# Kernel tuning notes

Hardware: AMD Instinct MI355X
Metric: run time of the kernel (lower is better)

Reference implementation:

```python
import jax, jax.numpy as jnp
import numpy as np

B, H, S, D = 4, 16, 1024, 64


def setup_inputs() -> dict:
    key = jax.random.key(0)
    kq, kk, kv, kw = jax.random.split(key, 4)
    xq = jax.random.normal(kq, (B, H, S, D), dtype=jnp.float32)
    xk = jax.random.normal(kk, (B, H, S, D), dtype=jnp.float32)
    xv = jax.random.normal(kv, (B, H, S, D), dtype=jnp.float32)
    # wpsm: nn.Linear(n_heads, n_heads, bias=False) weight, shape [H_out, H_in]
    bound = 1.0 / np.sqrt(H)
    W = jax.random.uniform(kw, (H, H), minval=-bound, maxval=bound, dtype=jnp.float32)
    return {"xq": xq, "xk": xk, "xv": xv, "W": W, "causal": 1}


def reference(xq, xk, xv, W, causal):
    head_dim = xq.shape[-1]
    sq, sk = xq.shape[-2], xk.shape[-2]
    # QK^T scaled: [B, H, Sq, Sk]
    scores = jnp.einsum("bhqd,bhkd->bhqk", xq, xk) * jax.lax.rsqrt(jnp.float32(head_dim))
    # head-mixing linear over head axis: mixed[b,g,q,k] = sum_h W[g,h] * scores[b,h,q,k]
    scores = jnp.einsum("gh,bhqk->bgqk", W, scores)
    if causal:
        mask = jnp.triu(jnp.full((sq, sk), -jnp.inf, dtype=scores.dtype), k=1)
        scores = scores + mask  # broadcast over [B, H]
    probs = jax.nn.softmax(scores.astype(jnp.float32), axis=-1).astype(xq.dtype)
    out = jnp.einsum("bhqk,bhkd->bhqd", probs, xv)
    return out.transpose(0, 2, 1, 3)  # [B, Sq, H, D]
```

## Files before the change

### kernel.cpp

```cpp
#include <hip/hip_runtime.h>
#include <math.h>

#define NB 4
#define HH 16
#define SS 1024
#define DD 64
#define NKST 16

typedef __attribute__((ext_vector_type(8))) short bf16x8;
typedef __attribute__((ext_vector_type(4))) float f32x4;

static __device__ __forceinline__ short f2bf(float f) {
    __bf16 h = (__bf16)f;
    return __builtin_bit_cast(short, h);
}
static __device__ __forceinline__ float bflo(int w) {
    return __builtin_bit_cast(float, (unsigned)w << 16);
}
static __device__ __forceinline__ float bfhi(int w) {
    return __builtin_bit_cast(float, (unsigned)w & 0xffff0000u);
}
static __device__ __forceinline__ float bfu(unsigned short u) {
    return __builtin_bit_cast(float, (unsigned)u << 16);
}
static __device__ __forceinline__ int pidx(int pos, int hp) {
    int s = ((pos >> 2) & 3) | (((pos >> 9) & 1) << 2);
    return pos * 8 + (hp ^ s);
}
static __device__ __forceinline__ int midx(int g, int loc, int x3) {
    return g * 512 + ((((loc >> 2) ^ x3) << 2) | (loc & 3));
}

static __device__ __forceinline__ bf16x8 load8_bf16(const float* p) {
    const float4* p4 = reinterpret_cast<const float4*>(p);
    float4 a = p4[0], b = p4[1];
    bf16x8 f;
    f[0]=f2bf(a.x); f[1]=f2bf(a.y); f[2]=f2bf(a.z); f[3]=f2bf(a.w);
    f[4]=f2bf(b.x); f[5]=f2bf(b.y); f[6]=f2bf(b.z); f[7]=f2bf(b.w);
    return f;
}

__global__ __launch_bounds__(256) void prep_kfrag(const float* __restrict__ xk,
                                                  short* __restrict__ kfr) {
    int c = blockIdx.x * 256 + threadIdx.x;
    int lane = c & 63, ds = (c >> 6) & 1, kt = (c >> 7) & 3;
    int kst = (c >> 9) & 15, h = (c >> 13) & 15, b = c >> 17;
    const float* src = xk + ((size_t)((b * HH + h) * SS) + kst * 64 + kt * 16 + (lane & 15)) * DD
                          + ds * 32 + (lane >> 4) * 8;
    *(reinterpret_cast<bf16x8*>(kfr) + c) = load8_bf16(src);
}

__global__ __launch_bounds__(256) void prep_vfrag(const float* __restrict__ xv,
                                                  short* __restrict__ vfr) {
    __shared__ float T[64][65];
    int tile = blockIdx.x;
    int t = threadIdx.x;
    const float* src = xv + ((size_t)(tile >> 4) * SS + (tile & 15) * 64) * DD;
    int row = t >> 2, col = (t & 3) * 16;
#pragma unroll
    for (int ii = 0; ii < 4; ++ii) {
        float4 v = *reinterpret_cast<const float4*>(src + row * DD + col + ii * 4);
        T[row][col + ii*4] = v.x; T[row][col + ii*4 + 1] = v.y;
        T[row][col + ii*4 + 2] = v.z; T[row][col + ii*4 + 3] = v.w;
    }
    __syncthreads();
#pragma unroll
    for (int jj = 0; jj < 2; ++jj) {
        int c2 = t * 2 + jj;
        int lane = c2 & 63, nt = (c2 >> 6) & 3, kc = (c2 >> 8) & 1;
        bf16x8 o;
#pragma unroll
        for (int i = 0; i < 8; ++i)
            o[i] = f2bf(T[kc * 32 + (lane >> 4) * 8 + i][nt * 16 + (lane & 15)]);
        *(reinterpret_cast<bf16x8*>(vfr) + (size_t)tile * 512 + c2) = o;
    }
}

__global__ __launch_bounds__(1024, 1) void hca_fused(
    const float* __restrict__ xq, const short* __restrict__ kfr,
    const short* __restrict__ vfr, const float* __restrict__ Wm,
    const int* __restrict__ causalp, unsigned short* __restrict__ ppO,
    float2* __restrict__ ppml)
{
    __shared__ int Pbuf[8192];
    __shared__ int Mbuf[8192];

    const int tid  = threadIdx.x;
    const int lane = tid & 63;
    const int w    = tid >> 6;
    const int l15  = lane & 15;
    const int lg   = lane >> 4;

    const int bid  = blockIdx.x;
    const int b    = bid & 3;
    const int pp   = (bid >> 2) & 31;
    const int kpar = (bid >> 7) & 1;

    const int causal = causalp[0];
    const int hp = w & 7;
    const int kh = w >> 3;
    const int g  = w;

    const float LOG2E = 1.44269504088896f;

    bf16x8 wt = {0,0,0,0,0,0,0,0};
    if (lg < 2) {
#pragma unroll
        for (int ii = 0; ii < 8; ++ii)
            wt[ii] = f2bf(Wm[l15 * 16 + lg * 8 + ii] * 0.125f * LOG2E);
    }

    const short* vb0 = vfr + (size_t)(b * HH + g) * NKST * 8 * 512 + lane * 8;
    const short* kb0 = kfr + (size_t)(b * HH + 2 * hp) * NKST * 8 * 512 + lane * 8;

#pragma unroll 1
    for (int seg = 0; seg < 2; ++seg) {
        const int qt = seg ? pp : 63 - pp;
        const int q0 = qt << 4;
        const int pairIdx = b * 64 + qt;

        bf16x8 qf[2][2];
#pragma unroll
        for (int hi = 0; hi < 2; ++hi) {
            const float* qp = xq + ((size_t)(b * HH + 2 * hp + hi) * SS + q0 + l15) * DD + lg * 8;
#pragma unroll
            for (int ds = 0; ds < 2; ++ds) qf[hi][ds] = load8_bf16(qp + ds * 32);
        }

        f32x4 oacc[4];
#pragma unroll
        for (int nt = 0; nt < 4; ++nt) oacc[nt] = (f32x4){0.f, 0.f, 0.f, 0.f};
        float mrun = -INFINITY, lrun = 0.f;

        const int nkf = causal ? ((q0 + 16 + 63) >> 6) : NKST;

#pragma unroll 1
        for (int kst = kpar; kst < nkf; kst += 2) {
            const int k0 = kst << 6;

            const short* kbase = kb0 + (size_t)kst * 8 * 512;
            __builtin_amdgcn_s_setprio(1);
#pragma unroll
            for (int kt2 = 0; kt2 < 2; ++kt2) {
                const int kt = kh * 2 + kt2;
                f32x4 a0 = (f32x4){0.f,0.f,0.f,0.f}, a1 = a0;
#pragma unroll
                for (int ds = 0; ds < 2; ++ds) {
                    bf16x8 kfa = *reinterpret_cast<const bf16x8*>(kbase + (kt*2 + ds) * 512);
                    bf16x8 kfb = *reinterpret_cast<const bf16x8*>(kbase + (NKST*8 + kt*2 + ds) * 512);
                    a0 = __builtin_amdgcn_mfma_f32_16x16x32_bf16(qf[0][ds], kfa, a0, 0, 0, 0);
                    a1 = __builtin_amdgcn_mfma_f32_16x16x32_bf16(qf[1][ds], kfb, a1, 0, 0, 0);
                }
#pragma unroll
                for (int r = 0; r < 4; ++r) {
                    int pos = (lg * 4 + r) * 64 + kt * 16 + l15;
                    int pk = (int)(unsigned short)f2bf(a0[r]) | ((int)(unsigned short)f2bf(a1[r]) << 16);
                    Pbuf[pidx(pos, hp)] = pk;
                }
            }
            __builtin_amdgcn_s_setprio(0);

            const short* vbase = vb0 + (size_t)kst * 8 * 512;
            bf16x8 vf[8];
#pragma unroll
            for (int kc = 0; kc < 2; ++kc)
#pragma unroll
                for (int nt = 0; nt < 4; ++nt)
                    vf[kc * 4 + nt] = *reinterpret_cast<const bf16x8*>(vbase + (kc*4 + nt) * 512);

            __syncthreads();

#pragma unroll
            for (int m = 0; m < 4; ++m) {
                const int c = w * 4 + m;
                const int pos = c * 16 + l15;
                int4 ia = {0, 0, 0, 0};
                if (lg < 2) {
                    ia.x = Pbuf[pidx(pos, lg * 4 + 0)];
                    ia.y = Pbuf[pidx(pos, lg * 4 + 1)];
                    ia.z = Pbuf[pidx(pos, lg * 4 + 2)];
                    ia.w = Pbuf[pidx(pos, lg * 4 + 3)];
                }
                bf16x8 A = __builtin_bit_cast(bf16x8, ia);
                f32x4 cc = (f32x4){0.f, 0.f, 0.f, 0.f};
                cc = __builtin_amdgcn_mfma_f32_16x16x32_bf16(A, wt, cc, 0, 0, 0);
                int loc = w * 32 + (c & 3) * 8 + lg * 2;
                int x3 = (w + l15) & 7;
                int u0 = (int)(unsigned short)f2bf(cc[0]) | ((int)(unsigned short)f2bf(cc[1]) << 16);
                int u1 = (int)(unsigned short)f2bf(cc[2]) | ((int)(unsigned short)f2bf(cc[3]) << 16);
                *reinterpret_cast<int2*>(&Mbuf[midx(l15, loc, x3)]) = make_int2(u0, u1);
            }
            __syncthreads();

            const int x3r = (l15 + g) & 7;
            int4 rA = *reinterpret_cast<const int4*>(&Mbuf[midx(g, l15 * 32 + lg * 4, x3r)]);
            int4 rB = *reinterpret_cast<const int4*>(&Mbuf[midx(g, l15 * 32 + 16 + lg * 4, x3r)]);

            float sm[16];
#pragma unroll
            for (int jj = 0; jj < 4; ++jj) {
                sm[2*jj]     = bflo(rA[jj]);  sm[2*jj + 1] = bfhi(rA[jj]);
                sm[8 + 2*jj] = bflo(rB[jj]);  sm[9 + 2*jj] = bfhi(rB[jj]);
            }
            if (causal && kst == nkf - 1) {
#pragma unroll
                for (int jj = 0; jj < 16; ++jj) {
                    int kk = (jj < 8) ? (lg * 8 + jj) : (32 + lg * 8 + (jj - 8));
                    if (k0 + kk > q0 + l15) sm[jj] = -INFINITY;
                }
            }

            float mx[4];
#pragma unroll
            for (int t = 0; t < 4; ++t)
                mx[t] = fmaxf(fmaxf(sm[4*t], sm[4*t+1]), fmaxf(sm[4*t+2], sm[4*t+3]));
            float mt = fmaxf(fmaxf(mx[0], mx[1]), fmaxf(mx[2], mx[3]));
            mt = fmaxf(mt, __shfl_xor(mt, 16));
            mt = fmaxf(mt, __shfl_xor(mt, 32));

            if (__any(mt > mrun + 8.0f)) {
                float mnew = fmaxf(mrun, mt);
                float scl = __builtin_amdgcn_exp2f(mrun - mnew);
                mrun = mnew;
                lrun *= scl;
                int scli = __builtin_bit_cast(int, scl);
#pragma unroll
                for (int r = 0; r < 4; ++r) {
                    int v = __builtin_amdgcn_ds_bpermute((lg * 4 + r) * 4, scli);
                    float s = __builtin_bit_cast(float, v);
#pragma unroll
                    for (int nt = 0; nt < 4; ++nt) oacc[nt][r] *= s;
                }
            }

#pragma unroll
            for (int jj = 0; jj < 16; ++jj) sm[jj] = __builtin_amdgcn_exp2f(sm[jj] - mrun);
            float s0 = ((sm[0]+sm[1]) + (sm[2]+sm[3])) + ((sm[4]+sm[5]) + (sm[6]+sm[7]));
            float s1 = ((sm[8]+sm[9]) + (sm[10]+sm[11])) + ((sm[12]+sm[13]) + (sm[14]+sm[15]));
            lrun += s0 + s1;

            int paw[8];
#pragma unroll
            for (int t = 0; t < 8; ++t)
                paw[t] = (int)(unsigned short)f2bf(sm[2*t]) | ((int)(unsigned short)f2bf(sm[2*t+1]) << 16);
            bf16x8 pa0 = __builtin_bit_cast(bf16x8, *(int4*)&paw[0]);
            bf16x8 pa1 = __builtin_bit_cast(bf16x8, *(int4*)&paw[4]);

            __builtin_amdgcn_s_setprio(1);
#pragma unroll
            for (int nt = 0; nt < 4; ++nt) {
                oacc[nt] = __builtin_amdgcn_mfma_f32_16x16x32_bf16(pa0, vf[nt], oacc[nt], 0, 0, 0);
                oacc[nt] = __builtin_amdgcn_mfma_f32_16x16x32_bf16(pa1, vf[4 + nt], oacc[nt], 0, 0, 0);
            }
            __builtin_amdgcn_s_setprio(0);
        }

        float lt = lrun;
        lt += __shfl_xor(lt, 16);
        lt += __shfl_xor(lt, 32);
        if (lg == 0)
            ppml[(((size_t)pairIdx * 2 + kpar) * 16 + g) * 16 + l15] = make_float2(mrun, lt);
        float rl = (lt > 0.f) ? (1.0f / lt) : 0.f;
        int rli = __builtin_bit_cast(int, rl);
        size_t obase = (((size_t)pairIdx * 2 + kpar) * 16 + g) * 1024;
#pragma unroll
        for (int r = 0; r < 4; ++r) {
            int v = __builtin_amdgcn_ds_bpermute((lg * 4 + r) * 4, rli);
            float linv = __builtin_bit_cast(float, v);
            int q = lg * 4 + r;
#pragma unroll
            for (int nt = 0; nt < 4; ++nt)
                ppO[obase + q * 64 + nt * 16 + l15] =
                    (unsigned short)f2bf(oacc[nt][r] * linv);
        }
        __syncthreads();
    }
}

__global__ __launch_bounds__(256) void hca_combine(
    const unsigned short* __restrict__ ppO, const float2* __restrict__ ppml,
    float* __restrict__ out)
{
    const int pairIdx = blockIdx.x;
    const int b = pairIdx >> 6, qt = pairIdx & 63;
    const int t = threadIdx.x;
    const int g = t >> 4, dc = t & 15;

    const size_t o0 = (((size_t)pairIdx * 2 + 0) * 16 + g) * 1024;
    const size_t o1 = (((size_t)pairIdx * 2 + 1) * 16 + g) * 1024;
    const float2* ml0p = ppml + (((size_t)pairIdx * 2 + 0) * 16 + g) * 16;
    const float2* ml1p = ppml + (((size_t)pairIdx * 2 + 1) * 16 + g) * 16;

#pragma unroll 4
    for (int q = 0; q < 16; ++q) {
        float2 ml0 = ml0p[q], ml1 = ml1p[q];
        float ms = fmaxf(ml0.x, ml1.x);
        float w0 = ml0.y * exp2f(ml0.x - ms);
        float w1 = ml1.y * exp2f(ml1.x - ms);
        float rs = 1.0f / (w0 + w1);
        float a0 = w0 * rs, a1 = w1 * rs;
        ushort4 u0 = *reinterpret_cast<const ushort4*>(ppO + o0 + q * 64 + dc * 4);
        ushort4 u1 = *reinterpret_cast<const ushort4*>(ppO + o1 + q * 64 + dc * 4);
        float4 res;
        res.x = a0 * bfu(u0.x) + a1 * bfu(u1.x);
        res.y = a0 * bfu(u0.y) + a1 * bfu(u1.y);
        res.z = a0 * bfu(u0.z) + a1 * bfu(u1.z);
        res.w = a0 * bfu(u0.w) + a1 * bfu(u1.w);
        *reinterpret_cast<float4*>(out + (((size_t)b * SS + qt * 16 + q) * HH + g) * DD + dc * 4) = res;
    }
}

extern "C" void kernel_launch(void* const* d_in, const int* in_sizes, int n_in,
                              void* d_out, int out_size, void* d_ws, size_t ws_size,
                              hipStream_t stream) {
    const float* xq = (const float*)d_in[0];
    const float* xk = (const float*)d_in[1];
    const float* xv = (const float*)d_in[2];
    const float* Wm = (const float*)d_in[3];
    const int* causal = (const int*)d_in[4];
    float* out = (float*)d_out;

    short* vfr = (short*)d_ws;
    short* kfr = vfr + (size_t)NB * HH * SS * DD;
    unsigned short* ppO = (unsigned short*)(kfr + (size_t)NB * HH * SS * DD);
    float2* ppml = (float2*)(ppO + (size_t)512 * 16 * 1024);

    prep_kfrag<<<2048, 256, 0, stream>>>(xk, kfr);
    prep_vfrag<<<NB * HH * NKST, 256, 0, stream>>>(xv, vfr);

    hca_fused<<<256, 1024, 0, stream>>>(xq, kfr, vfr, Wm, causal, ppO, ppml);
    hca_combine<<<256, 256, 0, stream>>>(ppO, ppml, out);
}
```

Before: 78.42 us.

## Merge K/V prep kernels and software-prefetch K fragments across loop iterations

Folds the two preprocessing kernels into one launch that branches on block index, which removes one kernel launch and its gap. In the main fused kernel, the K fragments for the next key step are loaded into registers before the current step's softmax and PV work, so global load latency overlaps with compute. V fragment loads are split into two halves, with the second half issued after the second barrier to shorten live ranges. The change adds register pressure in a kernel capped at 1024 threads per block, and the last iteration issues a redundant reload.

```diff
diff --git a/kernel.cpp b/kernel.cpp
--- a/kernel.cpp
+++ b/kernel.cpp
@@ -40,39 +40,41 @@
     return f;
 }
 
-__global__ __launch_bounds__(256) void prep_kfrag(const float* __restrict__ xk,
-                                                  short* __restrict__ kfr) {
-    int c = blockIdx.x * 256 + threadIdx.x;
-    int lane = c & 63, ds = (c >> 6) & 1, kt = (c >> 7) & 3;
-    int kst = (c >> 9) & 15, h = (c >> 13) & 15, b = c >> 17;
-    const float* src = xk + ((size_t)((b * HH + h) * SS) + kst * 64 + kt * 16 + (lane & 15)) * DD
-                          + ds * 32 + (lane >> 4) * 8;
-    *(reinterpret_cast<bf16x8*>(kfr) + c) = load8_bf16(src);
-}
-
-__global__ __launch_bounds__(256) void prep_vfrag(const float* __restrict__ xv,
-                                                  short* __restrict__ vfr) {
+__global__ __launch_bounds__(256) void prep_all(const float* __restrict__ xk,
+                                                short* __restrict__ kfr,
+                                                const float* __restrict__ xv,
+                                                short* __restrict__ vfr) {
     __shared__ float T[64][65];
-    int tile = blockIdx.x;
-    int t = threadIdx.x;
-    const float* src = xv + ((size_t)(tile >> 4) * SS + (tile & 15) * 64) * DD;
-    int row = t >> 2, col = (t & 3) * 16;
-#pragma unroll
-    for (int ii = 0; ii < 4; ++ii) {
-        float4 v = *reinterpret_cast<const float4*>(src + row * DD + col + ii * 4);
-        T[row][col + ii*4] = v.x; T[row][col + ii*4 + 1] = v.y;
-        T[row][col + ii*4 + 2] = v.z; T[row][col + ii*4 + 3] = v.w;
-    }
-    __syncthreads();
-#pragma unroll
-    for (int jj = 0; jj < 2; ++jj) {
-        int c2 = t * 2 + jj;
-        int lane = c2 & 63, nt = (c2 >> 6) & 3, kc = (c2 >> 8) & 1;
-        bf16x8 o;
-#pragma unroll
-        for (int i = 0; i < 8; ++i)
-            o[i] = f2bf(T[kc * 32 + (lane >> 4) * 8 + i][nt * 16 + (lane & 15)]);
-        *(reinterpret_cast<bf16x8*>(vfr) + (size_t)tile * 512 + c2) = o;
+    const int bid = blockIdx.x;
+    const int t = threadIdx.x;
+    if (bid < 2048) {
+        int c = bid * 256 + t;
+        int lane = c & 63, ds = (c >> 6) & 1, kt = (c >> 7) & 3;
+        int kst = (c >> 9) & 15, h = (c >> 13) & 15, b = c >> 17;
+        const float* src = xk + ((size_t)((b * HH + h) * SS) + kst * 64 + kt * 16 + (lane & 15)) * DD
+                              + ds * 32 + (lane >> 4) * 8;
+        *(reinterpret_cast<bf16x8*>(kfr) + c) = load8_bf16(src);
+    } else {
+        int tile = bid - 2048;
+        const float* src = xv + ((size_t)(tile >> 4) * SS + (tile & 15) * 64) * DD;
+        int row = t >> 2, col = (t & 3) * 16;
+#pragma unroll
+        for (int ii = 0; ii < 4; ++ii) {
+            float4 v = *reinterpret_cast<const float4*>(src + row * DD + col + ii * 4);
+            T[row][col + ii*4] = v.x; T[row][col + ii*4 + 1] = v.y;
+            T[row][col + ii*4 + 2] = v.z; T[row][col + ii*4 + 3] = v.w;
+        }
+        __syncthreads();
+#pragma unroll
+        for (int jj = 0; jj < 2; ++jj) {
+            int c2 = t * 2 + jj;
+            int lane = c2 & 63, nt = (c2 >> 6) & 3, kc = (c2 >> 8) & 1;
+            bf16x8 o;
+#pragma unroll
+            for (int i = 0; i < 8; ++i)
+                o[i] = f2bf(T[kc * 32 + (lane >> 4) * 8 + i][nt * 16 + (lane & 15)]);
+            *(reinterpret_cast<bf16x8*>(vfr) + (size_t)tile * 512 + c2) = o;
+        }
     }
 }
 
@@ -134,11 +136,23 @@
 
         const int nkf = causal ? ((q0 + 16 + 63) >> 6) : NKST;
 
+        bf16x8 kA[2][2], kB[2][2];
+        {
+            const short* kbase = kb0 + (size_t)kpar * 8 * 512;
+#pragma unroll
+            for (int kt2 = 0; kt2 < 2; ++kt2)
+#pragma unroll
+                for (int ds = 0; ds < 2; ++ds) {
+                    const int kt = kh * 2 + kt2;
+                    kA[kt2][ds] = *reinterpret_cast<const bf16x8*>(kbase + (kt*2 + ds) * 512);
+                    kB[kt2][ds] = *reinterpret_cast<const bf16x8*>(kbase + (NKST*8 + kt*2 + ds) * 512);
+                }
+        }
+
 #pragma unroll 1
         for (int kst = kpar; kst < nkf; kst += 2) {
             const int k0 = kst << 6;
 
-            const short* kbase = kb0 + (size_t)kst * 8 * 512;
             __builtin_amdgcn_s_setprio(1);
 #pragma unroll
             for (int kt2 = 0; kt2 < 2; ++kt2) {
@@ -146,10 +160,8 @@
                 f32x4 a0 = (f32x4){0.f,0.f,0.f,0.f}, a1 = a0;
 #pragma unroll
                 for (int ds = 0; ds < 2; ++ds) {
-                    bf16x8 kfa = *reinterpret_cast<const bf16x8*>(kbase + (kt*2 + ds) * 512);
-                    bf16x8 kfb = *reinterpret_cast<const bf16x8*>(kbase + (NKST*8 + kt*2 + ds) * 512);
-                    a0 = __builtin_amdgcn_mfma_f32_16x16x32_bf16(qf[0][ds], kfa, a0, 0, 0, 0);
-                    a1 = __builtin_amdgcn_mfma_f32_16x16x32_bf16(qf[1][ds], kfb, a1, 0, 0, 0);
+                    a0 = __builtin_amdgcn_mfma_f32_16x16x32_bf16(qf[0][ds], kA[kt2][ds], a0, 0, 0, 0);
+                    a1 = __builtin_amdgcn_mfma_f32_16x16x32_bf16(qf[1][ds], kB[kt2][ds], a1, 0, 0, 0);
                 }
 #pragma unroll
                 for (int r = 0; r < 4; ++r) {
@@ -160,13 +172,23 @@
             }
             __builtin_amdgcn_s_setprio(0);
 
+            {
+                const int kstn = (kst + 2 < nkf) ? (kst + 2) : kst;
+                const short* kbase = kb0 + (size_t)kstn * 8 * 512;
+#pragma unroll
+                for (int kt2 = 0; kt2 < 2; ++kt2)
+#pragma unroll
+                    for (int ds = 0; ds < 2; ++ds) {
+                        const int kt = kh * 2 + kt2;
+                        kA[kt2][ds] = *reinterpret_cast<const bf16x8*>(kbase + (kt*2 + ds) * 512);
+                        kB[kt2][ds] = *reinterpret_cast<const bf16x8*>(kbase + (NKST*8 + kt*2 + ds) * 512);
+                    }
+            }
             const short* vbase = vb0 + (size_t)kst * 8 * 512;
-            bf16x8 vf[8];
-#pragma unroll
-            for (int kc = 0; kc < 2; ++kc)
-#pragma unroll
-                for (int nt = 0; nt < 4; ++nt)
-                    vf[kc * 4 + nt] = *reinterpret_cast<const bf16x8*>(vbase + (kc*4 + nt) * 512);
+            bf16x8 vf0[4];
+#pragma unroll
+            for (int nt = 0; nt < 4; ++nt)
+                vf0[nt] = *reinterpret_cast<const bf16x8*>(vbase + nt * 512);
 
             __syncthreads();
 
@@ -192,6 +214,11 @@
             }
             __syncthreads();
 
+            bf16x8 vf1[4];
+#pragma unroll
+            for (int nt = 0; nt < 4; ++nt)
+                vf1[nt] = *reinterpret_cast<const bf16x8*>(vbase + (4 + nt) * 512);
+
             const int x3r = (l15 + g) & 7;
             int4 rA = *reinterpret_cast<const int4*>(&Mbuf[midx(g, l15 * 32 + lg * 4, x3r)]);
             int4 rB = *reinterpret_cast<const int4*>(&Mbuf[midx(g, l15 * 32 + 16 + lg * 4, x3r)]);
@@ -248,10 +275,11 @@
 
             __builtin_amdgcn_s_setprio(1);
 #pragma unroll
-            for (int nt = 0; nt < 4; ++nt) {
-                oacc[nt] = __builtin_amdgcn_mfma_f32_16x16x32_bf16(pa0, vf[nt], oacc[nt], 0, 0, 0);
-                oacc[nt] = __builtin_amdgcn_mfma_f32_16x16x32_bf16(pa1, vf[4 + nt], oacc[nt], 0, 0, 0);
-            }
+            for (int nt = 0; nt < 4; ++nt)
+                oacc[nt] = __builtin_amdgcn_mfma_f32_16x16x32_bf16(pa0, vf0[nt], oacc[nt], 0, 0, 0);
+#pragma unroll
+            for (int nt = 0; nt < 4; ++nt)
+                oacc[nt] = __builtin_amdgcn_mfma_f32_16x16x32_bf16(pa1, vf1[nt], oacc[nt], 0, 0, 0);
             __builtin_amdgcn_s_setprio(0);
         }
 
@@ -325,8 +353,7 @@
     unsigned short* ppO = (unsigned short*)(kfr + (size_t)NB * HH * SS * DD);
     float2* ppml = (float2*)(ppO + (size_t)512 * 16 * 1024);
 
-    prep_kfrag<<<2048, 256, 0, stream>>>(xk, kfr);
-    prep_vfrag<<<NB * HH * NKST, 256, 0, stream>>>(xv, vfr);
+    prep_all<<<2048 + NB * HH * NKST, 256, 0, stream>>>(xk, kfr, xv, vfr);
 
     hca_fused<<<256, 1024, 0, stream>>>(xq, kfr, vfr, Wm, causal, ppO, ppml);
     hca_combine<<<256, 256, 0, stream>>>(ppO, ppml, out);
```

Measured after the change: 124.6 us. 58.9% more time.

## Split fused attention grid per query tile and merge K/V prep kernels

Applied to the files above, without the earlier changes.

The main kernel now launches 512 blocks, each handling one query tile, instead of 256 blocks that each looped over a balanced pair of tiles. The min-occupancy hint in the launch bounds is dropped so more than one block may be resident per CU. The K and V fragment prep kernels are merged into a single launch that branches on block index, saving one launch. The PV MFMAs are regrouped into two separate loops. Per-block causal work is now uneven, so load balance depends on the hardware scheduler and on register and LDS pressure allowing two blocks per CU.

```diff
diff --git a/kernel.cpp b/kernel.cpp
--- a/kernel.cpp
+++ b/kernel.cpp
@@ -40,43 +40,45 @@
     return f;
 }
 
-__global__ __launch_bounds__(256) void prep_kfrag(const float* __restrict__ xk,
-                                                  short* __restrict__ kfr) {
-    int c = blockIdx.x * 256 + threadIdx.x;
-    int lane = c & 63, ds = (c >> 6) & 1, kt = (c >> 7) & 3;
-    int kst = (c >> 9) & 15, h = (c >> 13) & 15, b = c >> 17;
-    const float* src = xk + ((size_t)((b * HH + h) * SS) + kst * 64 + kt * 16 + (lane & 15)) * DD
-                          + ds * 32 + (lane >> 4) * 8;
-    *(reinterpret_cast<bf16x8*>(kfr) + c) = load8_bf16(src);
-}
-
-__global__ __launch_bounds__(256) void prep_vfrag(const float* __restrict__ xv,
-                                                  short* __restrict__ vfr) {
+__global__ __launch_bounds__(256) void prep_all(const float* __restrict__ xk,
+                                                short* __restrict__ kfr,
+                                                const float* __restrict__ xv,
+                                                short* __restrict__ vfr) {
     __shared__ float T[64][65];
-    int tile = blockIdx.x;
-    int t = threadIdx.x;
-    const float* src = xv + ((size_t)(tile >> 4) * SS + (tile & 15) * 64) * DD;
-    int row = t >> 2, col = (t & 3) * 16;
-#pragma unroll
-    for (int ii = 0; ii < 4; ++ii) {
-        float4 v = *reinterpret_cast<const float4*>(src + row * DD + col + ii * 4);
-        T[row][col + ii*4] = v.x; T[row][col + ii*4 + 1] = v.y;
-        T[row][col + ii*4 + 2] = v.z; T[row][col + ii*4 + 3] = v.w;
-    }
-    __syncthreads();
-#pragma unroll
-    for (int jj = 0; jj < 2; ++jj) {
-        int c2 = t * 2 + jj;
-        int lane = c2 & 63, nt = (c2 >> 6) & 3, kc = (c2 >> 8) & 1;
-        bf16x8 o;
-#pragma unroll
-        for (int i = 0; i < 8; ++i)
-            o[i] = f2bf(T[kc * 32 + (lane >> 4) * 8 + i][nt * 16 + (lane & 15)]);
-        *(reinterpret_cast<bf16x8*>(vfr) + (size_t)tile * 512 + c2) = o;
-    }
-}
-
-__global__ __launch_bounds__(1024, 1) void hca_fused(
+    const int bid = blockIdx.x;
+    const int t = threadIdx.x;
+    if (bid < 2048) {
+        int c = bid * 256 + t;
+        int lane = c & 63, ds = (c >> 6) & 1, kt = (c >> 7) & 3;
+        int kst = (c >> 9) & 15, h = (c >> 13) & 15, b = c >> 17;
+        const float* src = xk + ((size_t)((b * HH + h) * SS) + kst * 64 + kt * 16 + (lane & 15)) * DD
+                              + ds * 32 + (lane >> 4) * 8;
+        *(reinterpret_cast<bf16x8*>(kfr) + c) = load8_bf16(src);
+    } else {
+        int tile = bid - 2048;
+        const float* src = xv + ((size_t)(tile >> 4) * SS + (tile & 15) * 64) * DD;
+        int row = t >> 2, col = (t & 3) * 16;
+#pragma unroll
+        for (int ii = 0; ii < 4; ++ii) {
+            float4 v = *reinterpret_cast<const float4*>(src + row * DD + col + ii * 4);
+            T[row][col + ii*4] = v.x; T[row][col + ii*4 + 1] = v.y;
+            T[row][col + ii*4 + 2] = v.z; T[row][col + ii*4 + 3] = v.w;
+        }
+        __syncthreads();
+#pragma unroll
+        for (int jj = 0; jj < 2; ++jj) {
+            int c2 = t * 2 + jj;
+            int lane = c2 & 63, nt = (c2 >> 6) & 3, kc = (c2 >> 8) & 1;
+            bf16x8 o;
+#pragma unroll
+            for (int i = 0; i < 8; ++i)
+                o[i] = f2bf(T[kc * 32 + (lane >> 4) * 8 + i][nt * 16 + (lane & 15)]);
+            *(reinterpret_cast<bf16x8*>(vfr) + (size_t)tile * 512 + c2) = o;
+        }
+    }
+}
+
+__global__ __launch_bounds__(1024) void hca_fused(
     const float* __restrict__ xq, const short* __restrict__ kfr,
     const short* __restrict__ vfr, const float* __restrict__ Wm,
     const int* __restrict__ causalp, unsigned short* __restrict__ ppO,
@@ -93,8 +95,12 @@
 
     const int bid  = blockIdx.x;
     const int b    = bid & 3;
-    const int pp   = (bid >> 2) & 31;
-    const int kpar = (bid >> 7) & 1;
+    const int u    = (bid >> 2) & 63;
+    const int r    = (bid >> 8) & 1;
+    const int qt   = r ? u : 63 - u;
+    const int kpar = u & 1;
+    const int q0   = qt << 4;
+    const int pairIdx = b * 64 + qt;
 
     const int causal = causalp[0];
     const int hp = w & 7;
@@ -113,167 +119,160 @@
     const short* vb0 = vfr + (size_t)(b * HH + g) * NKST * 8 * 512 + lane * 8;
     const short* kb0 = kfr + (size_t)(b * HH + 2 * hp) * NKST * 8 * 512 + lane * 8;
 
+    bf16x8 qf[2][2];
+#pragma unroll
+    for (int hi = 0; hi < 2; ++hi) {
+        const float* qp = xq + ((size_t)(b * HH + 2 * hp + hi) * SS + q0 + l15) * DD + lg * 8;
+#pragma unroll
+        for (int ds = 0; ds < 2; ++ds) qf[hi][ds] = load8_bf16(qp + ds * 32);
+    }
+
+    f32x4 oacc[4];
+#pragma unroll
+    for (int nt = 0; nt < 4; ++nt) oacc[nt] = (f32x4){0.f, 0.f, 0.f, 0.f};
+    float mrun = -INFINITY, lrun = 0.f;
+
+    const int nkf = causal ? ((q0 + 16 + 63) >> 6) : NKST;
+
 #pragma unroll 1
-    for (int seg = 0; seg < 2; ++seg) {
-        const int qt = seg ? pp : 63 - pp;
-        const int q0 = qt << 4;
-        const int pairIdx = b * 64 + qt;
-
-        bf16x8 qf[2][2];
-#pragma unroll
-        for (int hi = 0; hi < 2; ++hi) {
-            const float* qp = xq + ((size_t)(b * HH + 2 * hp + hi) * SS + q0 + l15) * DD + lg * 8;
-#pragma unroll
-            for (int ds = 0; ds < 2; ++ds) qf[hi][ds] = load8_bf16(qp + ds * 32);
-        }
-
-        f32x4 oacc[4];
-#pragma unroll
-        for (int nt = 0; nt < 4; ++nt) oacc[nt] = (f32x4){0.f, 0.f, 0.f, 0.f};
-        float mrun = -INFINITY, lrun = 0.f;
-
-        const int nkf = causal ? ((q0 + 16 + 63) >> 6) : NKST;
-
-#pragma unroll 1
-        for (int kst = kpar; kst < nkf; kst += 2) {
-            const int k0 = kst << 6;
-
-            const short* kbase = kb0 + (size_t)kst * 8 * 512;
-            __builtin_amdgcn_s_setprio(1);
-#pragma unroll
-            for (int kt2 = 0; kt2 < 2; ++kt2) {
-                const int kt = kh * 2 + kt2;
-                f32x4 a0 = (f32x4){0.f,0.f,0.f,0.f}, a1 = a0;
-#pragma unroll
-                for (int ds = 0; ds < 2; ++ds) {
-                    bf16x8 kfa = *reinterpret_cast<const bf16x8*>(kbase + (kt*2 + ds) * 512);
-                    bf16x8 kfb = *reinterpret_cast<const bf16x8*>(kbase + (NKST*8 + kt*2 + ds) * 512);
-                    a0 = __builtin_amdgcn_mfma_f32_16x16x32_bf16(qf[0][ds], kfa, a0, 0, 0, 0);
-                    a1 = __builtin_amdgcn_mfma_f32_16x16x32_bf16(qf[1][ds], kfb, a1, 0, 0, 0);
-                }
-#pragma unroll
-                for (int r = 0; r < 4; ++r) {
-                    int pos = (lg * 4 + r) * 64 + kt * 16 + l15;
-                    int pk = (int)(unsigned short)f2bf(a0[r]) | ((int)(unsigned short)f2bf(a1[r]) << 16);
-                    Pbuf[pidx(pos, hp)] = pk;
-                }
-            }
-            __builtin_amdgcn_s_setprio(0);
-
-            const short* vbase = vb0 + (size_t)kst * 8 * 512;
-            bf16x8 vf[8];
-#pragma unroll
-            for (int kc = 0; kc < 2; ++kc)
-#pragma unroll
-                for (int nt = 0; nt < 4; ++nt)
-                    vf[kc * 4 + nt] = *reinterpret_cast<const bf16x8*>(vbase + (kc*4 + nt) * 512);
-
-            __syncthreads();
-
-#pragma unroll
-            for (int m = 0; m < 4; ++m) {
-                const int c = w * 4 + m;
-                const int pos = c * 16 + l15;
-                int4 ia = {0, 0, 0, 0};
-                if (lg < 2) {
-                    ia.x = Pbuf[pidx(pos, lg * 4 + 0)];
-                    ia.y = Pbuf[pidx(pos, lg * 4 + 1)];
-                    ia.z = Pbuf[pidx(pos, lg * 4 + 2)];
-                    ia.w = Pbuf[pidx(pos, lg * 4 + 3)];
-                }
-                bf16x8 A = __builtin_bit_cast(bf16x8, ia);
-                f32x4 cc = (f32x4){0.f, 0.f, 0.f, 0.f};
-                cc = __builtin_amdgcn_mfma_f32_16x16x32_bf16(A, wt, cc, 0, 0, 0);
-                int loc = w * 32 + (c & 3) * 8 + lg * 2;
-                int x3 = (w + l15) & 7;
-                int u0 = (int)(unsigned short)f2bf(cc[0]) | ((int)(unsigned short)f2bf(cc[1]) << 16);
-                int u1 = (int)(unsigned short)f2bf(cc[2]) | ((int)(unsigned short)f2bf(cc[3]) << 16);
-                *reinterpret_cast<int2*>(&Mbuf[midx(l15, loc, x3)]) = make_int2(u0, u1);
-            }
-            __syncthreads();
-
-            const int x3r = (l15 + g) & 7;
-            int4 rA = *reinterpret_cast<const int4*>(&Mbuf[midx(g, l15 * 32 + lg * 4, x3r)]);
-            int4 rB = *reinterpret_cast<const int4*>(&Mbuf[midx(g, l15 * 32 + 16 + lg * 4, x3r)]);
-
-            float sm[16];
-#pragma unroll
-            for (int jj = 0; jj < 4; ++jj) {
-                sm[2*jj]     = bflo(rA[jj]);  sm[2*jj + 1] = bfhi(rA[jj]);
-                sm[8 + 2*jj] = bflo(rB[jj]);  sm[9 + 2*jj] = bfhi(rB[jj]);
-            }
-            if (causal && kst == nkf - 1) {
-#pragma unroll
-                for (int jj = 0; jj < 16; ++jj) {
-                    int kk = (jj < 8) ? (lg * 8 + jj) : (32 + lg * 8 + (jj - 8));
-                    if (k0 + kk > q0 + l15) sm[jj] = -INFINITY;
-                }
-            }
-
-            float mx[4];
-#pragma unroll
-            for (int t = 0; t < 4; ++t)
-                mx[t] = fmaxf(fmaxf(sm[4*t], sm[4*t+1]), fmaxf(sm[4*t+2], sm[4*t+3]));
-            float mt = fmaxf(fmaxf(mx[0], mx[1]), fmaxf(mx[2], mx[3]));
-            mt = fmaxf(mt, __shfl_xor(mt, 16));
-            mt = fmaxf(mt, __shfl_xor(mt, 32));
-
-            if (__any(mt > mrun + 8.0f)) {
-                float mnew = fmaxf(mrun, mt);
-                float scl = __builtin_amdgcn_exp2f(mrun - mnew);
-                mrun = mnew;
-                lrun *= scl;
-                int scli = __builtin_bit_cast(int, scl);
-#pragma unroll
-                for (int r = 0; r < 4; ++r) {
-                    int v = __builtin_amdgcn_ds_bpermute((lg * 4 + r) * 4, scli);
-                    float s = __builtin_bit_cast(float, v);
-#pragma unroll
-                    for (int nt = 0; nt < 4; ++nt) oacc[nt][r] *= s;
-                }
-            }
-
-#pragma unroll
-            for (int jj = 0; jj < 16; ++jj) sm[jj] = __builtin_amdgcn_exp2f(sm[jj] - mrun);
-            float s0 = ((sm[0]+sm[1]) + (sm[2]+sm[3])) + ((sm[4]+sm[5]) + (sm[6]+sm[7]));
-            float s1 = ((sm[8]+sm[9]) + (sm[10]+sm[11])) + ((sm[12]+sm[13]) + (sm[14]+sm[15]));
-            lrun += s0 + s1;
-
-            int paw[8];
-#pragma unroll
-            for (int t = 0; t < 8; ++t)
-                paw[t] = (int)(unsigned short)f2bf(sm[2*t]) | ((int)(unsigned short)f2bf(sm[2*t+1]) << 16);
-            bf16x8 pa0 = __builtin_bit_cast(bf16x8, *(int4*)&paw[0]);
-            bf16x8 pa1 = __builtin_bit_cast(bf16x8, *(int4*)&paw[4]);
-
-            __builtin_amdgcn_s_setprio(1);
-#pragma unroll
-            for (int nt = 0; nt < 4; ++nt) {
-                oacc[nt] = __builtin_amdgcn_mfma_f32_16x16x32_bf16(pa0, vf[nt], oacc[nt], 0, 0, 0);
-                oacc[nt] = __builtin_amdgcn_mfma_f32_16x16x32_bf16(pa1, vf[4 + nt], oacc[nt], 0, 0, 0);
-            }
-            __builtin_amdgcn_s_setprio(0);
-        }
-
-        float lt = lrun;
-        lt += __shfl_xor(lt, 16);
-        lt += __shfl_xor(lt, 32);
-        if (lg == 0)
-            ppml[(((size_t)pairIdx * 2 + kpar) * 16 + g) * 16 + l15] = make_float2(mrun, lt);
-        float rl = (lt > 0.f) ? (1.0f / lt) : 0.f;
-        int rli = __builtin_bit_cast(int, rl);
-        size_t obase = (((size_t)pairIdx * 2 + kpar) * 16 + g) * 1024;
-#pragma unroll
-        for (int r = 0; r < 4; ++r) {
-            int v = __builtin_amdgcn_ds_bpermute((lg * 4 + r) * 4, rli);
-            float linv = __builtin_bit_cast(float, v);
-            int q = lg * 4 + r;
+    for (int kst = kpar; kst < nkf; kst += 2) {
+        const int k0 = kst << 6;
+
+        const short* kbase = kb0 + (size_t)kst * 8 * 512;
+        __builtin_amdgcn_s_setprio(1);
+#pragma unroll
+        for (int kt2 = 0; kt2 < 2; ++kt2) {
+            const int kt = kh * 2 + kt2;
+            f32x4 a0 = (f32x4){0.f,0.f,0.f,0.f}, a1 = a0;
+#pragma unroll
+            for (int ds = 0; ds < 2; ++ds) {
+                bf16x8 kfa = *reinterpret_cast<const bf16x8*>(kbase + (kt*2 + ds) * 512);
+                bf16x8 kfb = *reinterpret_cast<const bf16x8*>(kbase + (NKST*8 + kt*2 + ds) * 512);
+                a0 = __builtin_amdgcn_mfma_f32_16x16x32_bf16(qf[0][ds], kfa, a0, 0, 0, 0);
+                a1 = __builtin_amdgcn_mfma_f32_16x16x32_bf16(qf[1][ds], kfb, a1, 0, 0, 0);
+            }
+#pragma unroll
+            for (int rr = 0; rr < 4; ++rr) {
+                int pos = (lg * 4 + rr) * 64 + kt * 16 + l15;
+                int pk = (int)(unsigned short)f2bf(a0[rr]) | ((int)(unsigned short)f2bf(a1[rr]) << 16);
+                Pbuf[pidx(pos, hp)] = pk;
+            }
+        }
+        __builtin_amdgcn_s_setprio(0);
+
+        const short* vbase = vb0 + (size_t)kst * 8 * 512;
+        bf16x8 vf[8];
+#pragma unroll
+        for (int kc = 0; kc < 2; ++kc)
 #pragma unroll
             for (int nt = 0; nt < 4; ++nt)
-                ppO[obase + q * 64 + nt * 16 + l15] =
-                    (unsigned short)f2bf(oacc[nt][r] * linv);
-        }
+                vf[kc * 4 + nt] = *reinterpret_cast<const bf16x8*>(vbase + (kc*4 + nt) * 512);
+
         __syncthreads();
+
+#pragma unroll
+        for (int m = 0; m < 4; ++m) {
+            const int c = w * 4 + m;
+            const int pos = c * 16 + l15;
+            int4 ia = {0, 0, 0, 0};
+            if (lg < 2) {
+                ia.x = Pbuf[pidx(pos, lg * 4 + 0)];
+                ia.y = Pbuf[pidx(pos, lg * 4 + 1)];
+                ia.z = Pbuf[pidx(pos, lg * 4 + 2)];
+                ia.w = Pbuf[pidx(pos, lg * 4 + 3)];
+            }
+            bf16x8 A = __builtin_bit_cast(bf16x8, ia);
+            f32x4 cc = (f32x4){0.f, 0.f, 0.f, 0.f};
+            cc = __builtin_amdgcn_mfma_f32_16x16x32_bf16(A, wt, cc, 0, 0, 0);
+            int loc = w * 32 + (c & 3) * 8 + lg * 2;
+            int x3 = (w + l15) & 7;
+            int u0 = (int)(unsigned short)f2bf(cc[0]) | ((int)(unsigned short)f2bf(cc[1]) << 16);
+            int u1 = (int)(unsigned short)f2bf(cc[2]) | ((int)(unsigned short)f2bf(cc[3]) << 16);
+            *reinterpret_cast<int2*>(&Mbuf[midx(l15, loc, x3)]) = make_int2(u0, u1);
+        }
+        __syncthreads();
+
+        const int x3r = (l15 + g) & 7;
+        int4 rA = *reinterpret_cast<const int4*>(&Mbuf[midx(g, l15 * 32 + lg * 4, x3r)]);
+        int4 rB = *reinterpret_cast<const int4*>(&Mbuf[midx(g, l15 * 32 + 16 + lg * 4, x3r)]);
+
+        float sm[16];
+#pragma unroll
+        for (int jj = 0; jj < 4; ++jj) {
+            sm[2*jj]     = bflo(rA[jj]);  sm[2*jj + 1] = bfhi(rA[jj]);
+            sm[8 + 2*jj] = bflo(rB[jj]);  sm[9 + 2*jj] = bfhi(rB[jj]);
+        }
+        if (causal && kst == nkf - 1) {
+#pragma unroll
+            for (int jj = 0; jj < 16; ++jj) {
+                int kk = (jj < 8) ? (lg * 8 + jj) : (32 + lg * 8 + (jj - 8));
+                if (k0 + kk > q0 + l15) sm[jj] = -INFINITY;
+            }
+        }
+
+        float mx[4];
+#pragma unroll
+        for (int t = 0; t < 4; ++t)
+            mx[t] = fmaxf(fmaxf(sm[4*t], sm[4*t+1]), fmaxf(sm[4*t+2], sm[4*t+3]));
+        float mt = fmaxf(fmaxf(mx[0], mx[1]), fmaxf(mx[2], mx[3]));
+        mt = fmaxf(mt, __shfl_xor(mt, 16));
+        mt = fmaxf(mt, __shfl_xor(mt, 32));
+
+        if (__any(mt > mrun + 8.0f)) {
+            float mnew = fmaxf(mrun, mt);
+            float scl = __builtin_amdgcn_exp2f(mrun - mnew);
+            mrun = mnew;
+            lrun *= scl;
+            int scli = __builtin_bit_cast(int, scl);
+#pragma unroll
+            for (int rr = 0; rr < 4; ++rr) {
+                int v = __builtin_amdgcn_ds_bpermute((lg * 4 + rr) * 4, scli);
+                float s = __builtin_bit_cast(float, v);
+#pragma unroll
+                for (int nt = 0; nt < 4; ++nt) oacc[nt][rr] *= s;
+            }
+        }
+
+#pragma unroll
+        for (int jj = 0; jj < 16; ++jj) sm[jj] = __builtin_amdgcn_exp2f(sm[jj] - mrun);
+        float s0 = ((sm[0]+sm[1]) + (sm[2]+sm[3])) + ((sm[4]+sm[5]) + (sm[6]+sm[7]));
+        float s1 = ((sm[8]+sm[9]) + (sm[10]+sm[11])) + ((sm[12]+sm[13]) + (sm[14]+sm[15]));
+        lrun += s0 + s1;
+
+        int paw[8];
+#pragma unroll
+        for (int t = 0; t < 8; ++t)
+            paw[t] = (int)(unsigned short)f2bf(sm[2*t]) | ((int)(unsigned short)f2bf(sm[2*t+1]) << 16);
+        bf16x8 pa0 = __builtin_bit_cast(bf16x8, *(int4*)&paw[0]);
+        bf16x8 pa1 = __builtin_bit_cast(bf16x8, *(int4*)&paw[4]);
+
+        __builtin_amdgcn_s_setprio(1);
+#pragma unroll
+        for (int nt = 0; nt < 4; ++nt)
+            oacc[nt] = __builtin_amdgcn_mfma_f32_16x16x32_bf16(pa0, vf[nt], oacc[nt], 0, 0, 0);
+#pragma unroll
+        for (int nt = 0; nt < 4; ++nt)
+            oacc[nt] = __builtin_amdgcn_mfma_f32_16x16x32_bf16(pa1, vf[4 + nt], oacc[nt], 0, 0, 0);
+        __builtin_amdgcn_s_setprio(0);
+    }
+
+    float lt = lrun;
+    lt += __shfl_xor(lt, 16);
+    lt += __shfl_xor(lt, 32);
+    if (lg == 0)
+        ppml[(((size_t)pairIdx * 2 + kpar) * 16 + g) * 16 + l15] = make_float2(mrun, lt);
+    float rl = (lt > 0.f) ? (1.0f / lt) : 0.f;
+    int rli = __builtin_bit_cast(int, rl);
+    size_t obase = (((size_t)pairIdx * 2 + kpar) * 16 + g) * 1024;
+#pragma unroll
+    for (int rr = 0; rr < 4; ++rr) {
+        int v = __builtin_amdgcn_ds_bpermute((lg * 4 + rr) * 4, rli);
+        float linv = __builtin_bit_cast(float, v);
+        int q = lg * 4 + rr;
+#pragma unroll
+        for (int nt = 0; nt < 4; ++nt)
+            ppO[obase + q * 64 + nt * 16 + l15] =
+                (unsigned short)f2bf(oacc[nt][rr] * linv);
     }
 }
 
@@ -325,9 +324,8 @@
     unsigned short* ppO = (unsigned short*)(kfr + (size_t)NB * HH * SS * DD);
     float2* ppml = (float2*)(ppO + (size_t)512 * 16 * 1024);
 
-    prep_kfrag<<<2048, 256, 0, stream>>>(xk, kfr);
-    prep_vfrag<<<NB * HH * NKST, 256, 0, stream>>>(xv, vfr);
-
-    hca_fused<<<256, 1024, 0, stream>>>(xq, kfr, vfr, Wm, causal, ppO, ppml);
+    prep_all<<<2048 + NB * HH * NKST, 256, 0, stream>>>(xk, kfr, xv, vfr);
+
+    hca_fused<<<512, 1024, 0, stream>>>(xq, kfr, vfr, Wm, causal, ppO, ppml);
     hca_combine<<<256, 256, 0, stream>>>(ppO, ppml, out);
 }
```

Result: slower. 80.13 us (+2.2%).
